# Performance work log

Measured on AMD Instinct MI355X. Metric: run time of the kernel, lower is better.

## Reference

```python
import jax, jax.numpy as jnp
import numpy as np

ROWS, CELLS = 64, 64          # B table rows, C cells per row
CN_LEN, CV_LEN = 8, 16        # tokens per column name / cell value
EMB, HID = 768, 3072
VOCAB, NTYPES = 32000, 8
N = ROWS * CELLS              # total cells
L_CV = CELLS * CV_LEN         # padded per-row cv length (max possible)


def setup_inputs() -> dict:
    key = jax.random.key(0)
    ks = jax.random.split(key, 12)
    cn_ids = jax.random.randint(ks[0], (N, CN_LEN), 0, VOCAB)
    # guarantee at least one valid token per column name (avoid div by zero)
    cn_mask = jax.random.randint(ks[1], (N, CN_LEN), 0, 2).at[:, 0].set(1)
    c_types = jax.random.randint(ks[2], (N,), 0, NTYPES)
    cv_ids = jax.random.randint(ks[3], (N, CV_LEN), 0, VOCAB)
    cv_mask = jax.random.randint(ks[4], (N, CV_LEN), 0, 2).astype(bool)
    s = 1.0 / np.sqrt(EMB)
    word_emb = jax.random.normal(ks[5], (VOCAB, EMB), jnp.float32) * 0.02
    type_emb = jax.random.normal(ks[6], (NTYPES, EMB), jnp.float32) * 0.02
    fuse_w1 = jax.random.normal(ks[7], (EMB, HID), jnp.float32) * s
    fuse_b1 = jnp.zeros((HID,), jnp.float32)
    fuse_w2 = jax.random.normal(ks[8], (HID, 1), jnp.float32) / np.sqrt(HID)
    fuse_b2 = jnp.zeros((1,), jnp.float32)
    gate_w1 = jax.random.normal(ks[9], (EMB, HID), jnp.float32) * s
    gate_b1 = jnp.zeros((HID,), jnp.float32)
    gate_w2 = jax.random.normal(ks[10], (HID, 1), jnp.float32) / np.sqrt(HID)
    gate_b2 = jnp.zeros((1,), jnp.float32)
    cls_weight = jax.random.uniform(ks[11], (1, 1, EMB), jnp.float32, -s, s)
    return dict(cn_ids=cn_ids, cn_mask=cn_mask, c_types=c_types, cv_ids=cv_ids,
                cv_mask=cv_mask, word_emb=word_emb, type_emb=type_emb,
                fuse_w1=fuse_w1, fuse_b1=fuse_b1, fuse_w2=fuse_w2, fuse_b2=fuse_b2,
                gate_w1=gate_w1, gate_b1=gate_b1, gate_w2=gate_w2, gate_b2=gate_b2,
                cls_weight=cls_weight)


def reference(cn_ids, cn_mask, c_types, cv_ids, cv_mask, word_emb, type_emb,
              fuse_w1, fuse_b1, fuse_w2, fuse_b2, gate_w1, gate_b1, gate_w2,
              gate_b2, cls_weight):
    # --- TabColumnEmb: masked avg of column-name tokens + datatype gate ---
    cn_we = word_emb[cn_ids]                                  # [N, cn_len, E]
    m = cn_mask.astype(cn_we.dtype)
    cn_e = (cn_we * m[..., None]).sum(1) / m.sum(1, keepdims=True)  # [N, E]
    dt_e = type_emb[c_types]                                  # [N, E]
    fgate = jax.nn.sigmoid(jax.nn.relu(dt_e @ fuse_w1 + fuse_b1) @ fuse_w2 + fuse_b2)
    cn_e = cn_e + dt_e * fgate
    # --- TabColumnValueEmb + RelationLink ---
    cv_e = word_emb[cv_ids]                                   # [N, cv_len, E]
    g = jax.nn.sigmoid(jax.nn.relu(cn_e @ gate_w1 + gate_b1) @ gate_w2 + gate_b2)
    linked = cv_e + (cn_e * g)[:, None, :]                    # [N, cv_len, E]
    # --- per-row ragged gather of masked cv tokens, zero-padded to L_CV ---
    cn_rows = cn_e.reshape(ROWS, CELLS, EMB)
    cv_rows = linked.reshape(ROWS, L_CV, EMB)
    mrows = cv_mask.reshape(ROWS, L_CV)
    pos = jnp.clip(jnp.cumsum(mrows.astype(jnp.int32), axis=1) - 1, 0, L_CV - 1)
    bidx = jnp.arange(ROWS)[:, None]
    mf = mrows[..., None].astype(cv_rows.dtype)
    # masked-out tokens contribute exact zeros -> pad_zeros semantics preserved
    cv_out = jnp.zeros((ROWS, L_CV, EMB), cv_rows.dtype).at[bidx, pos].add(cv_rows * mf)
    # --- TabCLSEmb: prepend learnable cls token ---
    cls = jnp.broadcast_to(cls_weight, (ROWS, 1, EMB))
    return jnp.concatenate([cls, cn_rows, cv_out], axis=1)    # [B, 1+C+L_CV, E]
```

## Files before the change

kernel.cpp:

```cpp
#include <hip/hip_runtime.h>
#include <hip/hip_bf16.h>

#define ROWS 64
#define CELLS 64
#define CN_LEN 8
#define CV_LEN 16
#define EMB 768
#define HID 3072
#define NCELL 4096
#define L_CV 1024
#define ROW_TOK 1089
#define HBLK 24

#define OFF_FPART 0UL
#define OFF_FGATE (OFF_FPART + 96UL*8*4)
#define OFF_GPART (OFF_FGATE + 64UL)
#define OFF_CNB   (OFF_GPART + 24UL*4096*4)
#define OFF_W1T   (OFF_CNB + 4096UL*768*2)
#define OFF_CST   (OFF_W1T + 3072UL*768*2)
#define OFF_CNT   (OFF_CST + 4096UL*4)

typedef __attribute__((ext_vector_type(8))) short bf16x8;
typedef __attribute__((ext_vector_type(4))) float f32x4;

static __device__ __forceinline__ short f2bf(float x) {
  unsigned u = __float_as_uint(x);
  unsigned r = (u + 0x7fffu + ((u >> 16) & 1u)) >> 16;
  return (short)r;
}

static __device__ __forceinline__ void gload16(const void* g, void* l) {
  __builtin_amdgcn_global_load_lds(
      (const __attribute__((address_space(1))) unsigned*)g,
      (__attribute__((address_space(3))) unsigned*)l, 16, 0, 0);
}

__global__ __launch_bounds__(512) void k_fgate_acc(
    const float* __restrict__ type_emb, const float* __restrict__ fuse_w1,
    const float* __restrict__ fuse_b1, const float* __restrict__ fuse_w2,
    float* __restrict__ fpart, const int* __restrict__ cv_mask,
    int* __restrict__ cstart, int* __restrict__ cnt) {
  __shared__ float te[8 * EMB];
  __shared__ float red[16][8][33];
  __shared__ int ssum[512];
  const int tid = threadIdx.x;
  if (blockIdx.x >= 96) {
    const int row = blockIdx.x - 96;
    const int base = row * L_CV + tid * 2;
    const int m0 = cv_mask[base], m1 = cv_mask[base + 1];
    const int s = m0 + m1;
    ssum[tid] = s;
    __syncthreads();
    for (int off = 1; off < 512; off <<= 1) {
      int v = (tid >= off) ? ssum[tid - off] : 0;
      __syncthreads();
      ssum[tid] += v;
      __syncthreads();
    }
    if ((tid & 7) == 0) cstart[row * CELLS + (tid >> 3)] = ssum[tid] - s;
    if (tid == 511) cnt[row] = ssum[511];
    return;
  }
  for (int i = tid; i < 8 * EMB; i += 512) te[i] = type_emb[i];
  __syncthreads();
  const int hl = tid & 31, eg = tid >> 5;
  const int h = blockIdx.x * 32 + hl;
  float acc[8] = {0.f, 0.f, 0.f, 0.f, 0.f, 0.f, 0.f, 0.f};
  const float* wp = fuse_w1 + h;
  #pragma unroll 4
  for (int i = 0; i < 48; i++) {
    const int e = eg * 48 + i;
    const float wv = wp[(size_t)e * HID];
    #pragma unroll
    for (int t = 0; t < 8; t++) acc[t] += te[t * EMB + e] * wv;
  }
  #pragma unroll
  for (int t = 0; t < 8; t++) red[eg][t][hl] = acc[t];
  __syncthreads();
  if (tid < 256) {
    const int t = tid >> 5, h2 = tid & 31;
    float a = fuse_b1[blockIdx.x * 32 + h2];
    #pragma unroll
    for (int e2 = 0; e2 < 16; e2++) a += red[e2][t][h2];
    float v = fmaxf(a, 0.f) * fuse_w2[blockIdx.x * 32 + h2];
    #pragma unroll
    for (int m = 1; m < 32; m <<= 1) v += __shfl_xor(v, m);
    if (h2 == 0) fpart[blockIdx.x * 8 + t] = v;
  }
}

__global__ __launch_bounds__(256) void k_w1t(const float* __restrict__ w1,
                                             short* __restrict__ w1t,
                                             const float* __restrict__ fpart,
                                             const float* __restrict__ fuse_b2,
                                             float* __restrict__ fgate) {
  __shared__ float tile[32][33];
  const int bx = blockIdx.x, by = blockIdx.y;
  const int tid = threadIdx.x;
  if (bx == 0 && by == 0 && tid < 8) {
    float s = fuse_b2[0];
    for (int j = 0; j < 96; j++) s += fpart[j * 8 + tid];
    fgate[tid] = 1.f / (1.f + expf(-s));
  }
  #pragma unroll
  for (int i = 0; i < 4; i++) {
    int idx = tid + i * 256;
    int rr = idx >> 5, cc = idx & 31;
    tile[rr][cc] = w1[(size_t)(by * 32 + rr) * HID + bx * 32 + cc];
  }
  __syncthreads();
  #pragma unroll
  for (int i = 0; i < 4; i++) {
    int idx = tid + i * 256;
    int rr = idx >> 5, cc = idx & 31;
    w1t[(size_t)(bx * 32 + rr) * EMB + by * 32 + cc] = f2bf(tile[cc][rr]);
  }
}

__global__ __launch_bounds__(192) void k_cn(
    const int* __restrict__ cn_ids, const int* __restrict__ cn_mask,
    const int* __restrict__ c_types, const float* __restrict__ word_emb,
    const float* __restrict__ type_emb, const float* __restrict__ cls_w,
    const float* __restrict__ fgate, short* __restrict__ cnb,
    float* __restrict__ out) {
  const int n = blockIdx.x, tid = threadIdx.x;
  const int row = n >> 6, cell = n & 63;
  const int* ids = cn_ids + n * CN_LEN;
  const int* msk = cn_mask + n * CN_LEN;
  float4 s = {0.f, 0.f, 0.f, 0.f};
  int cnt = 0;
  #pragma unroll
  for (int j = 0; j < CN_LEN; j++) {
    if (msk[j]) {
      cnt++;
      const float4 v = *(const float4*)&word_emb[(size_t)ids[j] * EMB + tid * 4];
      s.x += v.x; s.y += v.y; s.z += v.z; s.w += v.w;
    }
  }
  const float inv = 1.f / (float)cnt;
  const int t = c_types[n];
  const float fg = fgate[t];
  const float4 d = *(const float4*)&type_emb[(size_t)t * EMB + tid * 4];
  float4 c;
  c.x = s.x * inv + d.x * fg;
  c.y = s.y * inv + d.y * fg;
  c.z = s.z * inv + d.z * fg;
  c.w = s.w * inv + d.w * fg;
  short4 b;
  b.x = f2bf(c.x); b.y = f2bf(c.y); b.z = f2bf(c.z); b.w = f2bf(c.w);
  *(short4*)&cnb[(size_t)n * EMB + tid * 4] = b;
  *(float4*)&out[(size_t)row * ROW_TOK * EMB + (size_t)(1 + cell) * EMB + tid * 4] = c;
  if (cell == 0)
    *(float4*)&out[(size_t)row * ROW_TOK * EMB + tid * 4] =
        *(const float4*)&cls_w[tid * 4];
}

__global__ __launch_bounds__(256) void k_gate_gemm(
    const short* __restrict__ cnb, const short* __restrict__ w1t,
    const float* __restrict__ gate_b1, const float* __restrict__ gate_w2,
    float* __restrict__ gpart) {
  __shared__ short Asub[2][128 * 32];
  __shared__ short Bsub[2][128 * 32];
  const int tid = threadIdx.x;
  const int orig = blockIdx.x;
  const int wgid = (orig & 7) * 96 + (orig >> 3);
  const int bx = wgid & 31, by = wgid >> 5;
  const int n0 = bx * 128, h0 = by * 128;
  const int lane = tid & 63, w = tid >> 6;
  const int wr = w >> 1, wc = w & 1;
  const int r = lane & 15, g = lane >> 4;
  f32x4 acc[4][4];
  #pragma unroll
  for (int a = 0; a < 4; a++)
    #pragma unroll
    for (int b = 0; b < 4; b++) acc[a][b] = (f32x4)0.f;

  const int s0 = tid, s1 = tid + 256;
  const int ar0 = s0 >> 2, ac0 = (s0 & 3) * 8;
  const int ar1 = s1 >> 2, ac1 = (s1 & 3) * 8;
  const short* aB = cnb + (size_t)n0 * EMB;
  const short* bB = w1t + (size_t)h0 * EMB;

#define STAGE(buf, kk)                                                  \
  do {                                                                  \
    gload16(aB + (size_t)ar0 * EMB + (kk) + ac0, &Asub[buf][s0 * 8]);   \
    gload16(aB + (size_t)ar1 * EMB + (kk) + ac1, &Asub[buf][s1 * 8]);   \
    gload16(bB + (size_t)ar0 * EMB + (kk) + ac0, &Bsub[buf][s0 * 8]);   \
    gload16(bB + (size_t)ar1 * EMB + (kk) + ac1, &Bsub[buf][s1 * 8]);   \
  } while (0)

#define COMPUTE(buf)                                                          \
  do {                                                                        \
    bf16x8 fa[4], fb[4];                                                      \
    _Pragma("unroll")                                                         \
    for (int fm = 0; fm < 4; fm++)                                            \
      fa[fm] = *(const bf16x8*)&Asub[buf][(wr * 64 + fm * 16 + r) * 32 + g * 8]; \
    _Pragma("unroll")                                                         \
    for (int fn = 0; fn < 4; fn++)                                            \
      fb[fn] = *(const bf16x8*)&Bsub[buf][(wc * 64 + fn * 16 + r) * 32 + g * 8]; \
    _Pragma("unroll")                                                         \
    for (int fm = 0; fm < 4; fm++)                                            \
      _Pragma("unroll")                                                       \
      for (int fn = 0; fn < 4; fn++)                                          \
        acc[fm][fn] = __builtin_amdgcn_mfma_f32_16x16x32_bf16(                \
            fa[fm], fb[fn], acc[fm][fn], 0, 0, 0);                            \
  } while (0)

  STAGE(0, 0);
  __syncthreads();
  int cur = 0;
  for (int t = 0; t < 23; t++) {
    STAGE(cur ^ 1, (t + 1) * 32);
    COMPUTE(cur);
    __syncthreads();
    cur ^= 1;
  }
  COMPUTE(cur);

  float rsum[4][4];
  #pragma unroll
  for (int fm = 0; fm < 4; fm++) {
    float rs[4] = {0.f, 0.f, 0.f, 0.f};
    #pragma unroll
    for (int fn = 0; fn < 4; fn++) {
      const int h = h0 + wc * 64 + fn * 16 + r;
      const float bv = gate_b1[h];
      const float wv = gate_w2[h];
      #pragma unroll
      for (int q = 0; q < 4; q++)
        rs[q] += fmaxf(acc[fm][fn][q] + bv, 0.f) * wv;
    }
    #pragma unroll
    for (int q = 0; q < 4; q++) {
      #pragma unroll
      for (int m = 1; m < 16; m <<= 1) rs[q] += __shfl_xor(rs[q], m);
      rsum[fm][q] = rs[q];
    }
  }
  float* red = (float*)&Asub[0][0];
  __syncthreads();
  if (wc == 1 && r == 0) {
    #pragma unroll
    for (int fm = 0; fm < 4; fm++)
      #pragma unroll
      for (int q = 0; q < 4; q++)
        red[wr * 64 + fm * 16 + g * 4 + q] = rsum[fm][q];
  }
  __syncthreads();
  if (wc == 0 && r == 0) {
    #pragma unroll
    for (int fm = 0; fm < 4; fm++)
      #pragma unroll
      for (int q = 0; q < 4; q++) {
        const int i = wr * 64 + fm * 16 + g * 4 + q;
        gpart[(size_t)by * NCELL + n0 + i] = rsum[fm][q] + red[i];
      }
  }
#undef STAGE
#undef COMPUTE
}

__global__ __launch_bounds__(192) void k_cv_cell(
    const int* __restrict__ cv_ids, const int* __restrict__ cv_mask,
    const int* __restrict__ cstart, const int* __restrict__ cnt,
    const float* __restrict__ word_emb, const float* __restrict__ gpart,
    const float* __restrict__ gate_b2, float* __restrict__ out) {
  const int bx = blockIdx.x, row = blockIdx.y, tid = threadIdx.x;
  const size_t rbase = (size_t)row * ROW_TOK * EMB;
  if (bx >= CELLS) {
    const int base = cnt[row] + (bx - CELLS) * 8;
    const float4 z = {0.f, 0.f, 0.f, 0.f};
    #pragma unroll
    for (int i = 0; i < 8; i++) {
      const int k = base + i;
      if (k < L_CV)
        *(float4*)&out[rbase + (size_t)(65 + k) * EMB + tid * 4] = z;
    }
    return;
  }
  const int cell = bx;
  const int n = row * CELLS + cell;
  float sg = gate_b2[0];
  #pragma unroll
  for (int j = 0; j < HBLK; j++) sg += gpart[(size_t)j * NCELL + n];
  const float gg = 1.f / (1.f + expf(-sg));
  const float4 cn = *(const float4*)&out[rbase + (size_t)(1 + cell) * EMB + tid * 4];
  float4 cg;
  cg.x = cn.x * gg; cg.y = cn.y * gg; cg.z = cn.z * gg; cg.w = cn.w * gg;
  const int* ids = cv_ids + n * CV_LEN;
  const int* msk = cv_mask + n * CV_LEN;
  int pos = cstart[n];
  #pragma unroll
  for (int j = 0; j < CV_LEN; j++) {
    if (msk[j]) {
      const float4 we = *(const float4*)&word_emb[(size_t)ids[j] * EMB + tid * 4];
      float4 v;
      v.x = we.x + cg.x; v.y = we.y + cg.y; v.z = we.z + cg.z; v.w = we.w + cg.w;
      *(float4*)&out[rbase + (size_t)(65 + pos) * EMB + tid * 4] = v;
      pos++;
    }
  }
}

extern "C" void kernel_launch(void* const* d_in, const int* in_sizes, int n_in,
                              void* d_out, int out_size, void* d_ws, size_t ws_size,
                              hipStream_t stream) {
  const int* cn_ids    = (const int*)d_in[0];
  const int* cn_mask   = (const int*)d_in[1];
  const int* c_types   = (const int*)d_in[2];
  const int* cv_ids    = (const int*)d_in[3];
  const int* cv_mask   = (const int*)d_in[4];
  const float* word_emb = (const float*)d_in[5];
  const float* type_emb = (const float*)d_in[6];
  const float* fuse_w1  = (const float*)d_in[7];
  const float* fuse_b1  = (const float*)d_in[8];
  const float* fuse_w2  = (const float*)d_in[9];
  const float* fuse_b2  = (const float*)d_in[10];
  const float* gate_w1  = (const float*)d_in[11];
  const float* gate_b1  = (const float*)d_in[12];
  const float* gate_w2  = (const float*)d_in[13];
  const float* gate_b2  = (const float*)d_in[14];
  const float* cls_w    = (const float*)d_in[15];

  char* ws = (char*)d_ws;
  float* fpart = (float*)(ws + OFF_FPART);
  float* fgate = (float*)(ws + OFF_FGATE);
  float* gpart = (float*)(ws + OFF_GPART);
  short* cnb   = (short*)(ws + OFF_CNB);
  short* w1t   = (short*)(ws + OFF_W1T);
  int*   cst   = (int*)(ws + OFF_CST);
  int*   cntp  = (int*)(ws + OFF_CNT);
  float* out   = (float*)d_out;

  k_fgate_acc<<<160, 512, 0, stream>>>(type_emb, fuse_w1, fuse_b1, fuse_w2,
                                       fpart, cv_mask, cst, cntp);
  k_w1t<<<dim3(96, 24), 256, 0, stream>>>(gate_w1, w1t, fpart, fuse_b2, fgate);
  k_cn<<<NCELL, 192, 0, stream>>>(cn_ids, cn_mask, c_types, word_emb, type_emb,
                                  cls_w, fgate, cnb, out);
  k_gate_gemm<<<768, 256, 0, stream>>>(cnb, w1t, gate_b1, gate_w2, gpart);
  k_cv_cell<<<dim3(CELLS + 128, ROWS), 192, 0, stream>>>(cv_ids, cv_mask, cst,
                                                         cntp, word_emb, gpart,
                                                         gate_b2, out);
}
```

Before: 123.3 us.

## Fold w1 transpose into prep kernel, move zero-fill into gate GEMM launch

The gate_w1 transpose/bf16 conversion now runs as extra blocks of the first prep kernel, using larger 32x64 tiles, which removes one kernel launch. The fuse-gate sigmoid is computed per block inside k_cn from the partial sums instead of a separate reduction, so the fgate buffer goes away. Zero-padding of the cv output moves from k_cv_cell into extra blocks of the gate GEMM launch so it overlaps with GEMM work. The cost is some redundant per-block reduction in k_cn and mixed block roles that may hurt occupancy of the GEMM blocks.

```diff
diff --git a/kernel.cpp b/kernel.cpp
--- a/kernel.cpp
+++ b/kernel.cpp
@@ -11,10 +11,10 @@
 #define L_CV 1024
 #define ROW_TOK 1089
 #define HBLK 24
+#define FILL_CHUNKS 96
 
 #define OFF_FPART 0UL
-#define OFF_FGATE (OFF_FPART + 96UL*8*4)
-#define OFF_GPART (OFF_FGATE + 64UL)
+#define OFF_GPART (OFF_FPART + 96UL*8*4)
 #define OFF_CNB   (OFF_GPART + 24UL*4096*4)
 #define OFF_W1T   (OFF_CNB + 4096UL*768*2)
 #define OFF_CST   (OFF_W1T + 3072UL*768*2)
@@ -35,17 +35,36 @@
       (__attribute__((address_space(3))) unsigned*)l, 16, 0, 0);
 }
 
-__global__ __launch_bounds__(512) void k_fgate_acc(
+__global__ __launch_bounds__(512) void k_prep(
     const float* __restrict__ type_emb, const float* __restrict__ fuse_w1,
     const float* __restrict__ fuse_b1, const float* __restrict__ fuse_w2,
     float* __restrict__ fpart, const int* __restrict__ cv_mask,
-    int* __restrict__ cstart, int* __restrict__ cnt) {
-  __shared__ float te[8 * EMB];
-  __shared__ float red[16][8][33];
-  __shared__ int ssum[512];
+    int* __restrict__ cstart, int* __restrict__ cnt,
+    const float* __restrict__ w1, short* __restrict__ w1t) {
   const int tid = threadIdx.x;
-  if (blockIdx.x >= 96) {
-    const int row = blockIdx.x - 96;
+  const int b = blockIdx.x;
+  if (b >= 160) {
+    __shared__ float tile[32][65];
+    const int wb = b - 160;
+    const int ht = wb % 48, et = wb / 48;
+    #pragma unroll
+    for (int i = 0; i < 4; i++) {
+      const int idx = tid + i * 512;
+      const int rr = idx >> 6, cc = idx & 63;
+      tile[rr][cc] = w1[(size_t)(et * 32 + rr) * HID + ht * 64 + cc];
+    }
+    __syncthreads();
+    #pragma unroll
+    for (int i = 0; i < 4; i++) {
+      const int idx = tid + i * 512;
+      const int rr = idx >> 5, cc = idx & 31;
+      w1t[(size_t)(ht * 64 + rr) * EMB + et * 32 + cc] = f2bf(tile[cc][rr]);
+    }
+    return;
+  }
+  if (b >= 96) {
+    __shared__ int ssum[512];
+    const int row = b - 96;
     const int base = row * L_CV + tid * 2;
     const int m0 = cv_mask[base], m1 = cv_mask[base + 1];
     const int s = m0 + m1;
@@ -61,10 +80,12 @@
     if (tid == 511) cnt[row] = ssum[511];
     return;
   }
+  __shared__ float te[8 * EMB];
+  __shared__ float red[16][8][33];
   for (int i = tid; i < 8 * EMB; i += 512) te[i] = type_emb[i];
   __syncthreads();
   const int hl = tid & 31, eg = tid >> 5;
-  const int h = blockIdx.x * 32 + hl;
+  const int h = b * 32 + hl;
   float acc[8] = {0.f, 0.f, 0.f, 0.f, 0.f, 0.f, 0.f, 0.f};
   const float* wp = fuse_w1 + h;
   #pragma unroll 4
@@ -79,41 +100,13 @@
   __syncthreads();
   if (tid < 256) {
     const int t = tid >> 5, h2 = tid & 31;
-    float a = fuse_b1[blockIdx.x * 32 + h2];
+    float a = fuse_b1[b * 32 + h2];
     #pragma unroll
     for (int e2 = 0; e2 < 16; e2++) a += red[e2][t][h2];
-    float v = fmaxf(a, 0.f) * fuse_w2[blockIdx.x * 32 + h2];
+    float v = fmaxf(a, 0.f) * fuse_w2[b * 32 + h2];
     #pragma unroll
     for (int m = 1; m < 32; m <<= 1) v += __shfl_xor(v, m);
-    if (h2 == 0) fpart[blockIdx.x * 8 + t] = v;
-  }
-}
-
-__global__ __launch_bounds__(256) void k_w1t(const float* __restrict__ w1,
-                                             short* __restrict__ w1t,
-                                             const float* __restrict__ fpart,
-                                             const float* __restrict__ fuse_b2,
-                                             float* __restrict__ fgate) {
-  __shared__ float tile[32][33];
-  const int bx = blockIdx.x, by = blockIdx.y;
-  const int tid = threadIdx.x;
-  if (bx == 0 && by == 0 && tid < 8) {
-    float s = fuse_b2[0];
-    for (int j = 0; j < 96; j++) s += fpart[j * 8 + tid];
-    fgate[tid] = 1.f / (1.f + expf(-s));
-  }
-  #pragma unroll
-  for (int i = 0; i < 4; i++) {
-    int idx = tid + i * 256;
-    int rr = idx >> 5, cc = idx & 31;
-    tile[rr][cc] = w1[(size_t)(by * 32 + rr) * HID + bx * 32 + cc];
-  }
-  __syncthreads();
-  #pragma unroll
-  for (int i = 0; i < 4; i++) {
-    int idx = tid + i * 256;
-    int rr = idx >> 5, cc = idx & 31;
-    w1t[(size_t)(bx * 32 + rr) * EMB + by * 32 + cc] = f2bf(tile[cc][rr]);
+    if (h2 == 0) fpart[b * 8 + t] = v;
   }
 }
 
@@ -121,8 +114,8 @@
     const int* __restrict__ cn_ids, const int* __restrict__ cn_mask,
     const int* __restrict__ c_types, const float* __restrict__ word_emb,
     const float* __restrict__ type_emb, const float* __restrict__ cls_w,
-    const float* __restrict__ fgate, short* __restrict__ cnb,
-    float* __restrict__ out) {
+    const float* __restrict__ fpart, const float* __restrict__ fuse_b2,
+    short* __restrict__ cnb, float* __restrict__ out) {
   const int n = blockIdx.x, tid = threadIdx.x;
   const int row = n >> 6, cell = n & 63;
   const int* ids = cn_ids + n * CN_LEN;
@@ -139,7 +132,10 @@
   }
   const float inv = 1.f / (float)cnt;
   const int t = c_types[n];
-  const float fg = fgate[t];
+  float sg = fuse_b2[0];
+  #pragma unroll 8
+  for (int j = 0; j < 96; j++) sg += fpart[j * 8 + t];
+  const float fg = 1.f / (1.f + expf(-sg));
   const float4 d = *(const float4*)&type_emb[(size_t)t * EMB + tid * 4];
   float4 c;
   c.x = s.x * inv + d.x * fg;
@@ -158,10 +154,25 @@
 __global__ __launch_bounds__(256) void k_gate_gemm(
     const short* __restrict__ cnb, const short* __restrict__ w1t,
     const float* __restrict__ gate_b1, const float* __restrict__ gate_w2,
-    float* __restrict__ gpart) {
+    float* __restrict__ gpart, const int* __restrict__ cnt,
+    float* __restrict__ out) {
   __shared__ short Asub[2][128 * 32];
   __shared__ short Bsub[2][128 * 32];
   const int tid = threadIdx.x;
+  if (blockIdx.x >= 768) {
+    const int fb = blockIdx.x - 768;
+    const int row = fb / FILL_CHUNKS, chunk = fb % FILL_CHUNKS;
+    const int lim = cnt[row] * EMB;
+    const size_t base = (size_t)row * ROW_TOK * EMB + 65UL * EMB;
+    const float4 z = {0.f, 0.f, 0.f, 0.f};
+    const int c0 = chunk * 8192;
+    #pragma unroll
+    for (int i = 0; i < 8; i++) {
+      const int idx = c0 + i * 1024 + tid * 4;
+      if (idx >= lim) *(float4*)&out[base + idx] = z;
+    }
+    return;
+  }
   const int orig = blockIdx.x;
   const int wgid = (orig & 7) * 96 + (orig >> 3);
   const int bx = wgid & 31, by = wgid >> 5;
@@ -262,23 +273,11 @@
 
 __global__ __launch_bounds__(192) void k_cv_cell(
     const int* __restrict__ cv_ids, const int* __restrict__ cv_mask,
-    const int* __restrict__ cstart, const int* __restrict__ cnt,
-    const float* __restrict__ word_emb, const float* __restrict__ gpart,
-    const float* __restrict__ gate_b2, float* __restrict__ out) {
-  const int bx = blockIdx.x, row = blockIdx.y, tid = threadIdx.x;
+    const int* __restrict__ cstart, const float* __restrict__ word_emb,
+    const float* __restrict__ gpart, const float* __restrict__ gate_b2,
+    float* __restrict__ out) {
+  const int cell = blockIdx.x, row = blockIdx.y, tid = threadIdx.x;
   const size_t rbase = (size_t)row * ROW_TOK * EMB;
-  if (bx >= CELLS) {
-    const int base = cnt[row] + (bx - CELLS) * 8;
-    const float4 z = {0.f, 0.f, 0.f, 0.f};
-    #pragma unroll
-    for (int i = 0; i < 8; i++) {
-      const int k = base + i;
-      if (k < L_CV)
-        *(float4*)&out[rbase + (size_t)(65 + k) * EMB + tid * 4] = z;
-    }
-    return;
-  }
-  const int cell = bx;
   const int n = row * CELLS + cell;
   float sg = gate_b2[0];
   #pragma unroll
@@ -324,7 +323,6 @@
 
   char* ws = (char*)d_ws;
   float* fpart = (float*)(ws + OFF_FPART);
-  float* fgate = (float*)(ws + OFF_FGATE);
   float* gpart = (float*)(ws + OFF_GPART);
   short* cnb   = (short*)(ws + OFF_CNB);
   short* w1t   = (short*)(ws + OFF_W1T);
@@ -332,13 +330,12 @@
   int*   cntp  = (int*)(ws + OFF_CNT);
   float* out   = (float*)d_out;
 
-  k_fgate_acc<<<160, 512, 0, stream>>>(type_emb, fuse_w1, fuse_b1, fuse_w2,
-                                       fpart, cv_mask, cst, cntp);
-  k_w1t<<<dim3(96, 24), 256, 0, stream>>>(gate_w1, w1t, fpart, fuse_b2, fgate);
+  k_prep<<<160 + 1152, 512, 0, stream>>>(type_emb, fuse_w1, fuse_b1, fuse_w2,
+                                         fpart, cv_mask, cst, cntp, gate_w1, w1t);
   k_cn<<<NCELL, 192, 0, stream>>>(cn_ids, cn_mask, c_types, word_emb, type_emb,
-                                  cls_w, fgate, cnb, out);
-  k_gate_gemm<<<768, 256, 0, stream>>>(cnb, w1t, gate_b1, gate_w2, gpart);
-  k_cv_cell<<<dim3(CELLS + 128, ROWS), 192, 0, stream>>>(cv_ids, cv_mask, cst,
-                                                         cntp, word_emb, gpart,
-                                                         gate_b2, out);
-}
+                                  cls_w, fpart, fuse_b2, cnb, out);
+  k_gate_gemm<<<768 + ROWS * FILL_CHUNKS, 256, 0, stream>>>(
+      cnb, w1t, gate_b1, gate_w2, gpart, cntp, out);
+  k_cv_cell<<<dim3(CELLS, ROWS), 192, 0, stream>>>(cv_ids, cv_mask, cst,
+                                                   word_emb, gpart, gate_b2, out);
+}
```

Result: faster. 111.8 us (-9.3%).
